# Kernel optimization log

Hardware: AMD Instinct MI355X
Metric: run time of the kernel (lower is better)

## Reference

```python
import jax, jax.numpy as jnp
import numpy as np


def setup_inputs() -> dict:
    key = jax.random.key(0)
    ks = jax.random.split(key, 4)
    B, Tq, Tv, D = 8, 256, 512, 256  # decoder_dim = D = 256
    query = jax.random.normal(ks[0], (B, Tq, D), dtype=jnp.float32)
    value = jax.random.normal(ks[1], (B, Tv, D), dtype=jnp.float32)
    W1 = jax.random.normal(ks[2], (D, D), dtype=jnp.float32) * (1.0 / np.sqrt(D))
    b1 = jnp.zeros((D,), dtype=jnp.float32)
    W2 = jax.random.normal(ks[3], (D, D), dtype=jnp.float32) * (1.0 / np.sqrt(D))
    b2 = jnp.zeros((D,), dtype=jnp.float32)
    return {"query": query, "value": value, "W1": W1, "b1": b1, "W2": W2, "b2": b2}


def reference(query, value, W1, b1, W2, b2):
    # Dense projections: [B,Tq,D], [B,Tv,D]
    q = jnp.einsum('bqd,de->bqe', query, W1) + b1
    v = jnp.einsum('bvd,de->bve', value, W2) + b2
    # Additive (Bahdanau) score: broadcast tanh then reduce over feature dim
    # score: [B,Tq,Tv]  (intermediate [B,Tq,Tv,D] is the fusion target)
    score = jnp.tanh(q[:, :, None, :] + v[:, None, :, :]).sum(axis=-1)
    alignment = jax.nn.softmax(score, axis=-1)  # [B,Tq,Tv]
    context = jnp.einsum('bqv,bvd->bqd', alignment, value)  # [B,Tq,D]
    context = jnp.concatenate([context, query], axis=-1)  # [B,Tq,2D]
    alignment_t = jnp.transpose(alignment, (0, 2, 1))  # [B,Tv,Tq]
    return context, alignment_t
```

## Files before the change

### kernel.cpp

```cpp
#include <hip/hip_runtime.h>

#define B_  8
#define TQ  256
#define TV  512
#define DD  256

__device__ __forceinline__ float fast_exp2(float x) {
#if __has_builtin(__builtin_amdgcn_exp2f)
  return __builtin_amdgcn_exp2f(x);
#else
  return __exp2f(x);
#endif
}
__device__ __forceinline__ float fast_rcp(float x) {
#if __has_builtin(__builtin_amdgcn_rcpf)
  return __builtin_amdgcn_rcpf(x);
#else
  return 1.0f / x;
#endif
}

__global__ __launch_bounds__(256) void proj_fused(
    const float* __restrict__ query, const float* __restrict__ value,
    const float* __restrict__ W1, const float* __restrict__ b1,
    const float* __restrict__ W2, const float* __restrict__ b2,
    float* __restrict__ qp, float* __restrict__ vp, float scale) {
  __shared__ float As[64][33];
  __shared__ float Bs[64][64];
  const int t  = threadIdx.x;
  const int rt = blockIdx.x;
  const int bn = blockIdx.y * 64;

  const float* A; const float* W; const float* bias; float* out; int row0;
  if (rt < 64) { row0 = rt * 32;        A = query; W = W1; bias = b1; out = qp; }
  else         { row0 = (rt - 64) * 32; A = value; W = W2; bias = b2; out = vp; }

  const int tx = t & 15, ty = t >> 4;
  const int arow = t >> 3, acol = (t & 7) << 3;

  float acc[2][4] = {{0.f,0.f,0.f,0.f},{0.f,0.f,0.f,0.f}};

  for (int k0 = 0; k0 < 256; k0 += 64) {
    float4 a0 = *(const float4*)(A + (size_t)(row0 + arow) * DD + k0 + acol);
    float4 a1 = *(const float4*)(A + (size_t)(row0 + arow) * DD + k0 + acol + 4);
    As[acol + 0][arow] = a0.x; As[acol + 1][arow] = a0.y;
    As[acol + 2][arow] = a0.z; As[acol + 3][arow] = a0.w;
    As[acol + 4][arow] = a1.x; As[acol + 5][arow] = a1.y;
    As[acol + 6][arow] = a1.z; As[acol + 7][arow] = a1.w;
#pragma unroll
    for (int k = 0; k < 4; ++k) {
      const int id = (k << 8) + t;
      const int row = id >> 4, col4 = (id & 15) << 2;
      *(float4*)&Bs[row][col4] =
          *(const float4*)(W + (size_t)(k0 + row) * DD + bn + col4);
    }
    __syncthreads();
#pragma unroll 16
    for (int k = 0; k < 64; ++k) {
      float2 av = *(const float2*)&As[k][ty << 1];
      float4 bv = *(const float4*)&Bs[k][tx << 2];
      acc[0][0] = fmaf(av.x, bv.x, acc[0][0]); acc[0][1] = fmaf(av.x, bv.y, acc[0][1]);
      acc[0][2] = fmaf(av.x, bv.z, acc[0][2]); acc[0][3] = fmaf(av.x, bv.w, acc[0][3]);
      acc[1][0] = fmaf(av.y, bv.x, acc[1][0]); acc[1][1] = fmaf(av.y, bv.y, acc[1][1]);
      acc[1][2] = fmaf(av.y, bv.z, acc[1][2]); acc[1][3] = fmaf(av.y, bv.w, acc[1][3]);
    }
    __syncthreads();
  }

  float4 bvv = *(const float4*)&bias[bn + (tx << 2)];
#pragma unroll
  for (int r = 0; r < 2; ++r) {
    float4 o;
    o.x = fast_exp2(scale * (acc[r][0] + bvv.x));
    o.y = fast_exp2(scale * (acc[r][1] + bvv.y));
    o.z = fast_exp2(scale * (acc[r][2] + bvv.z));
    o.w = fast_exp2(scale * (acc[r][3] + bvv.w));
    *(float4*)(out + (size_t)(row0 + (ty << 1) + r) * DD + bn + (tx << 2)) = o;
  }
}

__global__ __launch_bounds__(512, 4) void attn_kernel(
    const float* __restrict__ qp, const float* __restrict__ vp,
    const float* __restrict__ value, const float* __restrict__ query,
    float* __restrict__ out1, float* __restrict__ out2) {
  __shared__ float vs[512 * 36];
  float* alg = vs;

  const int t    = threadIdx.x;
  const int lane = t & 63;
  const int wv   = t >> 6;
  const int bb   = blockIdx.x & 7;
  const int i0   = (blockIdx.x >> 3) << 2;
  const int jrow = (wv << 6) + lane;

  const float* vpb = vp + (size_t)bb * TV * DD;
  const float* qb  = qp + (size_t)(bb * TQ + i0) * DD;

  const int j0   = t >> 3;
  const int col4 = (t & 7) << 2;

  float acc[4] = {0.f, 0.f, 0.f, 0.f};

#pragma unroll 1
  for (int dc = 0; dc < 8; ++dc) {
    const int dbase = dc << 5;
#pragma unroll
    for (int k = 0; k < 8; ++k) {
      const int j = (k << 6) + j0;
      float4 x = *(const float4*)(vpb + (size_t)j * DD + dbase + col4);
      *(float4*)&vs[j * 36 + col4] = x;
    }
    __syncthreads();

#pragma unroll
    for (int d4 = 0; d4 < 8; ++d4) {
      float4 v4 = *(const float4*)&vs[jrow * 36 + (d4 << 2)];
#pragma unroll
      for (int i = 0; i < 4; ++i) {
        float4 q4 = *(const float4*)(qb + i * DD + dbase + (d4 << 2));
        float a = q4.x * v4.x, b = q4.y * v4.y;
        float c = q4.z * v4.z, d = q4.w * v4.w;
        float sab = a + b,  scd = c + d;
        float Q1 = fmaf(a, b, sab + 1.f);
        float Q2 = fmaf(c, d, scd + 1.f);
        float P1 = sab + 2.f, P2 = scd + 2.f;
        float N  = fmaf(P2, Q1, P1 * Q2);
        acc[i] = fmaf(N, fast_rcp(Q1 * Q2), acc[i]);
      }
    }
    __syncthreads();
  }

#pragma unroll
  for (int i = 0; i < 4; ++i) alg[(i << 9) + jrow] = acc[i];
  __syncthreads();

  if (wv < 4) {
    float s[8];
#pragma unroll
    for (int c = 0; c < 8; ++c) s[c] = alg[(wv << 9) + (c << 6) + lane];
    float mn = s[0];
#pragma unroll
    for (int c = 1; c < 8; ++c) mn = fminf(mn, s[c]);
#pragma unroll
    for (int m = 1; m < 64; m <<= 1) mn = fminf(mn, __shfl_xor(mn, m, 64));

    const float CC = 2.8853900817779268f;
    float p[8];
    float sum = 0.f;
#pragma unroll
    for (int c = 0; c < 8; ++c) { p[c] = fast_exp2(CC * (mn - s[c])); sum += p[c]; }
#pragma unroll
    for (int m = 1; m < 64; m <<= 1) sum += __shfl_xor(sum, m, 64);
    const float inv = fast_rcp(sum);
#pragma unroll
    for (int c = 0; c < 8; ++c) alg[(wv << 9) + (c << 6) + lane] = p[c] * inv;
  }
  __syncthreads();

  {
    const int j = t;
    float4 av = make_float4(alg[j], alg[512 + j], alg[1024 + j], alg[1536 + j]);
    *(float4*)(out2 + (size_t)(bb * TV + j) * TQ + i0) = av;
  }

  const int f  = t & 255;
  const int rp = t >> 8;
  float c0 = 0.f, c1 = 0.f;
  const float* vb = value + (size_t)bb * TV * DD;
  const float* a0p = &alg[((rp << 1) + 0) << 9];
  const float* a1p = &alg[((rp << 1) + 1) << 9];
#pragma unroll 2
  for (int j = 0; j < TV; j += 4) {
    float v0 = vb[(size_t)(j + 0) * DD + f];
    float v1 = vb[(size_t)(j + 1) * DD + f];
    float v2 = vb[(size_t)(j + 2) * DD + f];
    float v3 = vb[(size_t)(j + 3) * DD + f];
    float4 a0 = *(const float4*)&a0p[j];
    float4 a1 = *(const float4*)&a1p[j];
    c0 += a0.x * v0 + a0.y * v1 + a0.z * v2 + a0.w * v3;
    c1 += a1.x * v0 + a1.y * v1 + a1.z * v2 + a1.w * v3;
  }

  const int r0 = (rp << 1), r1 = r0 + 1;
  const float* qg = query + (size_t)(bb * TQ + i0) * DD;
  float* o = out1 + (size_t)(bb * TQ + i0) * (2 * DD);
  o[r0 * 512 + f] = c0; o[r0 * 512 + 256 + f] = qg[r0 * DD + f];
  o[r1 * 512 + f] = c1; o[r1 * 512 + 256 + f] = qg[r1 * DD + f];
}

extern "C" void kernel_launch(void* const* d_in, const int* in_sizes, int n_in,
                              void* d_out, int out_size, void* d_ws, size_t ws_size,
                              hipStream_t stream) {
  const float* query = (const float*)d_in[0];
  const float* value = (const float*)d_in[1];
  const float* W1    = (const float*)d_in[2];
  const float* b1    = (const float*)d_in[3];
  const float* W2    = (const float*)d_in[4];
  const float* b2    = (const float*)d_in[5];

  float* out1 = (float*)d_out;
  float* out2 = out1 + (size_t)B_ * TQ * 2 * DD;

  float* qp = (float*)d_ws;
  float* vp = qp + (size_t)B_ * TQ * DD;

  const float SC = 2.8853900817779268f;

  proj_fused<<<dim3(192, 4), 256, 0, stream>>>(query, value, W1, b1, W2, b2, qp, vp, SC);
  attn_kernel<<<dim3(B_ * (TQ / 4)), 512, 0, stream>>>(qp, vp, value, query, out1, out2);
}
```

Before: 147.6 us.

## Rework projection GEMM with 64x64 tiles, double-buffered LDS and swizzled A layout

```diff
diff --git a/kernel.cpp b/kernel.cpp
--- a/kernel.cpp
+++ b/kernel.cpp
@@ -25,57 +25,91 @@
     const float* __restrict__ W1, const float* __restrict__ b1,
     const float* __restrict__ W2, const float* __restrict__ b2,
     float* __restrict__ qp, float* __restrict__ vp, float scale) {
-  __shared__ float As[64][33];
-  __shared__ float Bs[64][64];
+  __shared__ float As[2][32][64];
+  __shared__ float Bs[2][32][64];
   const int t  = threadIdx.x;
   const int rt = blockIdx.x;
-  const int bn = blockIdx.y * 64;
+  const int bn = blockIdx.y << 6;
 
   const float* A; const float* W; const float* bias; float* out; int row0;
-  if (rt < 64) { row0 = rt * 32;        A = query; W = W1; bias = b1; out = qp; }
-  else         { row0 = (rt - 64) * 32; A = value; W = W2; bias = b2; out = vp; }
+  if (rt < 32) { row0 = rt << 6;        A = query; W = W1; bias = b1; out = qp; }
+  else         { row0 = (rt - 32) << 6; A = value; W = W2; bias = b2; out = vp; }
 
   const int tx = t & 15, ty = t >> 4;
-  const int arow = t >> 3, acol = (t & 7) << 3;
-
-  float acc[2][4] = {{0.f,0.f,0.f,0.f},{0.f,0.f,0.f,0.f}};
-
-  for (int k0 = 0; k0 < 256; k0 += 64) {
-    float4 a0 = *(const float4*)(A + (size_t)(row0 + arow) * DD + k0 + acol);
-    float4 a1 = *(const float4*)(A + (size_t)(row0 + arow) * DD + k0 + acol + 4);
-    As[acol + 0][arow] = a0.x; As[acol + 1][arow] = a0.y;
-    As[acol + 2][arow] = a0.z; As[acol + 3][arow] = a0.w;
-    As[acol + 4][arow] = a1.x; As[acol + 5][arow] = a1.y;
-    As[acol + 6][arow] = a1.z; As[acol + 7][arow] = a1.w;
-#pragma unroll
-    for (int k = 0; k < 4; ++k) {
-      const int id = (k << 8) + t;
-      const int row = id >> 4, col4 = (id & 15) << 2;
-      *(float4*)&Bs[row][col4] =
-          *(const float4*)(W + (size_t)(k0 + row) * DD + bn + col4);
-    }
-    __syncthreads();
-#pragma unroll 16
-    for (int k = 0; k < 64; ++k) {
-      float2 av = *(const float2*)&As[k][ty << 1];
-      float4 bv = *(const float4*)&Bs[k][tx << 2];
-      acc[0][0] = fmaf(av.x, bv.x, acc[0][0]); acc[0][1] = fmaf(av.x, bv.y, acc[0][1]);
-      acc[0][2] = fmaf(av.x, bv.z, acc[0][2]); acc[0][3] = fmaf(av.x, bv.w, acc[0][3]);
-      acc[1][0] = fmaf(av.y, bv.x, acc[1][0]); acc[1][1] = fmaf(av.y, bv.y, acc[1][1]);
-      acc[1][2] = fmaf(av.y, bv.z, acc[1][2]); acc[1][3] = fmaf(av.y, bv.w, acc[1][3]);
-    }
-    __syncthreads();
+  const int aar = t >> 3, aac = (t & 7) << 2;
+  const int bbr = t >> 4, bbc = (t & 15) << 2;
+
+  float4 ra[2], rb[2];
+
+#pragma unroll
+  for (int it = 0; it < 2; ++it) {
+    ra[it] = *(const float4*)(A + (size_t)(row0 + (it << 5) + aar) * DD + aac);
+    rb[it] = *(const float4*)(W + (size_t)((it << 4) + bbr) * DD + bn + bbc);
+  }
+#pragma unroll
+  for (int it = 0; it < 2; ++it) {
+    const int m = (it << 5) + aar;
+#pragma unroll
+    for (int c = 0; c < 4; ++c) {
+      const int k = aac + c;
+      As[0][k][m ^ (((k >> 2) & 7) << 2)] = (&ra[it].x)[c];
+    }
+    *(float4*)&Bs[0][(it << 4) + bbr][bbc] = rb[it];
+  }
+  __syncthreads();
+
+  float acc[4][4] = {{0.f,0.f,0.f,0.f},{0.f,0.f,0.f,0.f},
+                     {0.f,0.f,0.f,0.f},{0.f,0.f,0.f,0.f}};
+  int p = 0;
+
+  for (int k0 = 0; k0 < 256; k0 += 32) {
+    const bool more = (k0 + 32) < 256;
+    if (more) {
+#pragma unroll
+      for (int it = 0; it < 2; ++it) {
+        ra[it] = *(const float4*)(A + (size_t)(row0 + (it << 5) + aar) * DD + k0 + 32 + aac);
+        rb[it] = *(const float4*)(W + (size_t)(k0 + 32 + (it << 4) + bbr) * DD + bn + bbc);
+      }
+    }
+#pragma unroll
+    for (int k = 0; k < 32; ++k) {
+      float4 aq = *(const float4*)&As[p][k][(ty << 2) ^ (((k >> 2) & 7) << 2)];
+      float4 bq = *(const float4*)&Bs[p][k][tx << 2];
+      acc[0][0] = fmaf(aq.x, bq.x, acc[0][0]); acc[0][1] = fmaf(aq.x, bq.y, acc[0][1]);
+      acc[0][2] = fmaf(aq.x, bq.z, acc[0][2]); acc[0][3] = fmaf(aq.x, bq.w, acc[0][3]);
+      acc[1][0] = fmaf(aq.y, bq.x, acc[1][0]); acc[1][1] = fmaf(aq.y, bq.y, acc[1][1]);
+      acc[1][2] = fmaf(aq.y, bq.z, acc[1][2]); acc[1][3] = fmaf(aq.y, bq.w, acc[1][3]);
+      acc[2][0] = fmaf(aq.z, bq.x, acc[2][0]); acc[2][1] = fmaf(aq.z, bq.y, acc[2][1]);
+      acc[2][2] = fmaf(aq.z, bq.z, acc[2][2]); acc[2][3] = fmaf(aq.z, bq.w, acc[2][3]);
+      acc[3][0] = fmaf(aq.w, bq.x, acc[3][0]); acc[3][1] = fmaf(aq.w, bq.y, acc[3][1]);
+      acc[3][2] = fmaf(aq.w, bq.z, acc[3][2]); acc[3][3] = fmaf(aq.w, bq.w, acc[3][3]);
+    }
+    if (more) {
+      const int q = p ^ 1;
+#pragma unroll
+      for (int it = 0; it < 2; ++it) {
+        const int m = (it << 5) + aar;
+#pragma unroll
+        for (int c = 0; c < 4; ++c) {
+          const int k = aac + c;
+          As[q][k][m ^ (((k >> 2) & 7) << 2)] = (&ra[it].x)[c];
+        }
+        *(float4*)&Bs[q][(it << 4) + bbr][bbc] = rb[it];
+      }
+      __syncthreads();
+      p = q;
+    }
   }
 
   float4 bvv = *(const float4*)&bias[bn + (tx << 2)];
 #pragma unroll
-  for (int r = 0; r < 2; ++r) {
+  for (int r = 0; r < 4; ++r) {
     float4 o;
     o.x = fast_exp2(scale * (acc[r][0] + bvv.x));
     o.y = fast_exp2(scale * (acc[r][1] + bvv.y));
     o.z = fast_exp2(scale * (acc[r][2] + bvv.z));
     o.w = fast_exp2(scale * (acc[r][3] + bvv.w));
-    *(float4*)(out + (size_t)(row0 + (ty << 1) + r) * DD + bn + (tx << 2)) = o;
+    *(float4*)(out + (size_t)(row0 + (ty << 2) + r) * DD + bn + (tx << 2)) = o;
   }
 }
 
@@ -207,6 +241,6 @@
 
   const float SC = 2.8853900817779268f;
 
-  proj_fused<<<dim3(192, 4), 256, 0, stream>>>(query, value, W1, b1, W2, b2, qp, vp, SC);
+  proj_fused<<<dim3(96, 4), 256, 0, stream>>>(query, value, W1, b1, W2, b2, qp, vp, SC);
   attn_kernel<<<dim3(B_ * (TQ / 4)), 512, 0, stream>>>(qp, vp, value, query, out1, out2);
 }
```

Measured after the change: 149.3 us. No clear change (+1.2%).
